# Kernel optimization log

Hardware: AMD Instinct MI355X
Metric: run time of the kernel (lower is better)

## Reference

```python
import jax, jax.numpy as jnp
import numpy as np

NEG_INF = -9e15
ALPHA = 0.2  # LeakyReLU negative slope
OUT_FEATURES = 128


def setup_inputs() -> dict:
    key = jax.random.key(0)
    k1, k2, k3, k4 = jax.random.split(key, 4)
    B, N, F_in, F_out = 4, 4096, 256, OUT_FEATURES
    h = jax.random.normal(k1, (B, N, F_in), dtype=jnp.float32)
    adj = jax.random.randint(k2, (B, N, N), 0, 2, dtype=jnp.int32)
    W = jax.random.normal(k3, (F_in, F_out), dtype=jnp.float32) * 0.07
    a = jax.random.normal(k4, (2 * F_out, 1), dtype=jnp.float32) * 0.1
    return {"h": h, "adj": adj, "W": W, "a": a}


def reference(h, adj, W, a):
    # Wh: (B, N, F_out)
    Wh = jnp.einsum('bni,io->bno', h, W)
    a1 = a[:OUT_FEATURES, 0]   # (F_out,)
    a2 = a[OUT_FEATURES:, 0]   # (F_out,)
    Wh1 = Wh @ a1              # (B, N)
    Wh2 = Wh @ a2              # (B, N)
    e = Wh1[:, :, None] + Wh2[:, None, :]          # (B, N, N)
    e = jnp.where(e >= 0, e, ALPHA * e)             # LeakyReLU
    e = jnp.where(adj > 0, e, NEG_INF)              # adjacency mask
    attention = jax.nn.softmax(e, axis=-1)          # (B, N, N)
    # dropout omitted: reference runs in eval mode (training=False)
    h_prime = jnp.einsum('bnm,bmo->bno', attention, Wh)
    return jax.nn.elu(h_prime)  # concat=True
```

## Files before the change

kernel.cpp:

```cpp
#include <hip/hip_runtime.h>
#include <hip/hip_bf16.h>
#include <math.h>

typedef __attribute__((ext_vector_type(4))) float  f32x4;
typedef __attribute__((ext_vector_type(4))) int    i32x4;
typedef __attribute__((ext_vector_type(8))) short  s16x8;
typedef __attribute__((ext_vector_type(4))) short  s16x4;
typedef __attribute__((ext_vector_type(8))) __bf16 bf16x8;

#define LOG2E 1.4426950408889634f

__device__ __forceinline__ short f32_to_bf16_rne(float f) {
    unsigned u = __builtin_bit_cast(unsigned, f);
    u += 0x7fffu + ((u >> 16) & 1u);
    return (short)(u >> 16);
}
__device__ __forceinline__ int pack2_bf16(float f0, float f1) {
    unsigned u0 = __builtin_bit_cast(unsigned, f0) + 0x8000u;
    unsigned u1 = __builtin_bit_cast(unsigned, f1) + 0x8000u;
    return (int)((u0 >> 16) | (u1 & 0xffff0000u));
}
__device__ __forceinline__ bf16x8 as_bf16x8(s16x8 v) {
    return __builtin_bit_cast(bf16x8, v);
}
__device__ __forceinline__ bf16x8 as_bf16x8(i32x4 v) {
    return __builtin_bit_cast(bf16x8, v);
}

__global__ void k0_wt(const float* __restrict__ W, short* __restrict__ WT) {
    int g = blockIdx.x * 256 + threadIdx.x;
    int col = g >> 6;
    int k0 = (g & 63) * 4;
    s16x4 v;
    #pragma unroll
    for (int i = 0; i < 4; ++i) v[i] = f32_to_bf16_rne(W[(k0 + i) * 128 + col]);
    *(s16x4*)(WT + col * 256 + k0) = v;
}

__global__ __launch_bounds__(256, 2) void k1_gemm(
    const float* __restrict__ h, const float* __restrict__ a,
    const short* __restrict__ WT,
    short* __restrict__ WhT, float* __restrict__ Wh1p, float* __restrict__ Tp)
{
    int l = threadIdx.x & 63;
    int w = threadIdx.x >> 6;
    int gw = blockIdx.x * 4 + w;
    int r0 = gw * 16;
    int lm = l & 15, q = l >> 4;

    f32x4 acc[8];
    #pragma unroll
    for (int ct = 0; ct < 8; ++ct) acc[ct] = (f32x4)0.0f;

    const float* hrow = h + (long)(r0 + lm) * 256;
    for (int kb = 0; kb < 8; ++kb) {
        int kbase = kb * 32 + q * 8;
        f32x4 h0 = *(const f32x4*)(hrow + kbase);
        f32x4 h1 = *(const f32x4*)(hrow + kbase + 4);
        s16x8 af;
        #pragma unroll
        for (int j = 0; j < 4; ++j) af[j] = f32_to_bf16_rne(h0[j]);
        #pragma unroll
        for (int j = 0; j < 4; ++j) af[4 + j] = f32_to_bf16_rne(h1[j]);
        bf16x8 afb = as_bf16x8(af);
        #pragma unroll
        for (int ct = 0; ct < 8; ++ct) {
            s16x8 bf = *(const s16x8*)(WT + (ct * 16 + lm) * 256 + kbase);
            acc[ct] = __builtin_amdgcn_mfma_f32_16x16x32_bf16(afb, as_bf16x8(bf), acc[ct], 0, 0, 0);
        }
    }

    int b = r0 >> 12;
    int nb = r0 & 4095;
    float p1[4] = {0.f, 0.f, 0.f, 0.f}, p2[4] = {0.f, 0.f, 0.f, 0.f};
    #pragma unroll
    for (int ct = 0; ct < 8; ++ct) {
        int col = ct * 16 + lm;
        float a1c = a[col], a2c = a[128 + col];
        s16x4 vv;
        #pragma unroll
        for (int r = 0; r < 4; ++r) {
            float v = acc[ct][r];
            p1[r] += v * a1c;
            p2[r] += v * a2c;
            vv[r] = f32_to_bf16_rne(v);
        }
        *(s16x4*)(WhT + ((long)(b * 128 + col) * 4096 + nb + q * 4)) = vv;
    }
    #pragma unroll
    for (int off = 1; off < 16; off <<= 1) {
        #pragma unroll
        for (int r = 0; r < 4; ++r) {
            p1[r] += __shfl_xor(p1[r], off);
            p2[r] += __shfl_xor(p2[r], off);
        }
    }
    if (lm == 0) {
        #pragma unroll
        for (int r = 0; r < 4; ++r) {
            int row = r0 + q * 4 + r;
            Wh1p[row] = LOG2E * p1[r];
            Tp[row]   = LOG2E * p2[r];
        }
    }
}

__global__ void k2_tmax(const float* __restrict__ Tp, float* __restrict__ Tmax) {
    __shared__ float red[256];
    int b = blockIdx.x, t = threadIdx.x;
    float mx = -1e30f;
    for (int i = 0; i < 16; ++i) mx = fmaxf(mx, Tp[b * 4096 + t + i * 256]);
    red[t] = mx;
    __syncthreads();
    for (int s = 128; s > 0; s >>= 1) {
        if (t < s) red[t] = fmaxf(red[t], red[t + s]);
        __syncthreads();
    }
    if (t == 0) Tmax[b] = red[0];
}

template <int SPLIT>
__global__ __launch_bounds__(256, 2) void k3_attn(
    const int* __restrict__ adj, const short* __restrict__ WhT,
    const float* __restrict__ Wh1p, const float* __restrict__ Tp,
    const float* __restrict__ Tmax,
    float* __restrict__ U, float* __restrict__ Z)
{
    const int MSLICE = 4096 / SPLIT;
    const int MTILES = MSLICE / 128;
    __shared__ __align__(16) short tile[2][128 * 128];
    __shared__ __align__(16) float tps[4096 / SPLIT];

    int l = threadIdx.x & 63, w = threadIdx.x >> 6;
    int lm = l & 15, q = l >> 4;
    int bid = blockIdx.x;
    int mh = bid & (SPLIT - 1);
    int rg = (bid / SPLIT) & 63;
    int b  = bid / (SPLIT * 64);
    int n0 = rg * 64;
    int mbase = mh * MSLICE;

    int n_lane = n0 + w * 16 + lm;
    float sp = Wh1p[b * 4096 + n_lane];
    float xm = sp + Tmax[b];
    float Mrow = fmaxf(xm, 0.2f * xm);

    const int*   adjrow = adj + ((long)(b * 4096 + n_lane) << 12) + q * 8;
    const short* whtb   = WhT + (long)b * 128 * 4096;
    const float* tpsq   = tps + q * 8;

    {
        const float* tg = Tp + b * 4096 + mbase;
        int i0 = threadIdx.x * 4;
        *(f32x4*)(tps + i0)        = *(const f32x4*)(tg + i0);
        *(f32x4*)(tps + i0 + 1024) = *(const f32x4*)(tg + i0 + 1024);
    }

    f32x4 acc[8];
    #pragma unroll
    for (int ct = 0; ct < 8; ++ct) acc[ct] = (f32x4)0.0f;
    float z = 0.0f;

    auto stage = [&](short* dst, int m0) {
        int colw = w * 32;
        #pragma unroll
        for (int j = 0; j < 8; ++j) {
            int cb = colw + j * 4;
            int col = cb + q;
            int gch = lm ^ (col & 7);
            const short* gp = whtb + (long)col * 4096 + m0 + gch * 8;
            __builtin_amdgcn_global_load_lds(
                (const __attribute__((address_space(1))) void*)gp,
                (__attribute__((address_space(3))) void*)(dst + cb * 128), 16, 0, 0);
        }
    };
    auto ldadj = [&](i32x4* aj, int m0) {
        #pragma unroll
        for (int ks = 0; ks < 4; ++ks) {
            aj[2 * ks]     = *(const i32x4*)(adjrow + m0 + ks * 32);
            aj[2 * ks + 1] = *(const i32x4*)(adjrow + m0 + ks * 32 + 4);
        }
    };
    auto compute = [&](const short* buf, const i32x4* aj, int mrel) {
        #pragma unroll
        for (int ks = 0; ks < 4; ++ks) {
            f32x4 t0 = *(const f32x4*)(tpsq + mrel + ks * 32);
            f32x4 t1 = *(const f32x4*)(tpsq + mrel + ks * 32 + 4);
            i32x4 pk;
            float zs = 0.0f;
            #pragma unroll
            for (int half = 0; half < 2; ++half) {
                i32x4 a4 = aj[2 * ks + half];
                f32x4 t4 = half ? t1 : t0;
                float wv[4];
                #pragma unroll
                for (int j = 0; j < 4; ++j) {
                    float y = sp + t4[j];
                    float e = fmaxf(y, 0.2f * y) - Mrow;
                    float v = __builtin_amdgcn_exp2f(e);
                    v = (a4[j] != 0) ? v : 0.0f;
                    zs += v; wv[j] = v;
                }
                pk[half * 2]     = pack2_bf16(wv[0], wv[1]);
                pk[half * 2 + 1] = pack2_bf16(wv[2], wv[3]);
            }
            z += zs;
            bf16x8 ab = as_bf16x8(pk);
            #pragma unroll
            for (int ct = 0; ct < 8; ++ct) {
                int col = ct * 16 + lm;
                int pos = (ks * 4 + q) ^ (col & 7);
                s16x8 bf = *(const s16x8*)(buf + col * 128 + pos * 8);
                acc[ct] = __builtin_amdgcn_mfma_f32_16x16x32_bf16(ab, as_bf16x8(bf), acc[ct], 0, 0, 0);
            }
        }
    };

    i32x4 ajA[8], ajB[8];
    stage(tile[0], mbase);
    ldadj(ajA, mbase);
    __syncthreads();

    #pragma unroll 1
    for (int t = 0; t < MTILES; t += 2) {
        int r1 = (t + 1) & (MTILES - 1);
        stage(tile[1], mbase + r1 * 128);
        ldadj(ajB, mbase + r1 * 128);
        __builtin_amdgcn_sched_barrier(0);
        compute(tile[0], ajA, t * 128);
        __syncthreads();
        int r2 = (t + 2) & (MTILES - 1);
        stage(tile[0], mbase + r2 * 128);
        ldadj(ajA, mbase + r2 * 128);
        __builtin_amdgcn_sched_barrier(0);
        compute(tile[1], ajB, r1 * 128);
        __syncthreads();
    }

    z += __shfl_xor(z, 16);
    z += __shfl_xor(z, 32);

    int slice = b * SPLIT + mh;
    if (l < 16) Z[slice * 4096 + n0 + w * 16 + lm] = z;
    float* ub = U + ((long)slice * 4096 + n0 + w * 16) * 128;
    #pragma unroll
    for (int ct = 0; ct < 8; ++ct) {
        int col = ct * 16 + lm;
        #pragma unroll
        for (int r = 0; r < 4; ++r)
            ub[(q * 4 + r) * 128 + col] = acc[ct][r];
    }
}

__global__ void k4_combine(const float* __restrict__ U, const float* __restrict__ Z,
                           float* __restrict__ out) {
    long g = (long)blockIdx.x * 256 + threadIdx.x;
    long off = g * 4;
    long nf = off >> 7;
    int b = (int)(nf >> 12), n = (int)(nf & 4095), col = (int)(off & 127);
    long base0 = ((long)(b * 2) * 4096 + n) * 128 + col;
    f32x4 u0 = *(const f32x4*)(U + base0);
    f32x4 u1 = *(const f32x4*)(U + base0 + (long)4096 * 128);
    float zz = Z[(b * 2) * 4096 + n] + Z[(b * 2 + 1) * 4096 + n];
    f32x4 v;
    #pragma unroll
    for (int i = 0; i < 4; ++i) {
        float x = (u0[i] + u1[i]) / zz;
        v[i] = (x > 0.f) ? x : (expf(x) - 1.0f);
    }
    *(f32x4*)(out + off) = v;
}

extern "C" void kernel_launch(void* const* d_in, const int* in_sizes, int n_in,
                              void* d_out, int out_size, void* d_ws, size_t ws_size,
                              hipStream_t stream) {
    const float* h   = (const float*)d_in[0];
    const int*   adj = (const int*)d_in[1];
    const float* W   = (const float*)d_in[2];
    const float* a   = (const float*)d_in[3];
    float* out = (float*)d_out;

    char* ws = (char*)d_ws;
    short* WhT  = (short*)ws;
    short* WT   = (short*)(ws + 4194304);
    float* Wh1p = (float*)(ws + 4259840);
    float* Tp   = (float*)(ws + 4325376);
    float* Tmax = (float*)(ws + 4390912);
    float* U    = (float*)(ws + 4391168);
    float* Z    = (float*)(ws + 4391168 + 16777216);

    k0_wt<<<32, 256, 0, stream>>>(W, WT);
    k1_gemm<<<256, 256, 0, stream>>>(h, a, WT, WhT, Wh1p, Tp);
    k2_tmax<<<4, 256, 0, stream>>>(Tp, Tmax);
    k3_attn<2><<<512, 256, 0, stream>>>(adj, WhT, Wh1p, Tp, Tmax, U, Z);
    k4_combine<<<2048, 256, 0, stream>>>(U, Z, out);
    (void)in_sizes; (void)n_in; (void)out_size; (void)ws_size;
}
```

Baseline: 404.7 us.

## Pre-pack adjacency matrix into bitmasks before attention kernel

```diff
diff --git a/kernel.cpp b/kernel.cpp
--- a/kernel.cpp
+++ b/kernel.cpp
@@ -4,6 +4,7 @@
 
 typedef __attribute__((ext_vector_type(4))) float  f32x4;
 typedef __attribute__((ext_vector_type(4))) int    i32x4;
+typedef __attribute__((ext_vector_type(4))) unsigned u32x4;
 typedef __attribute__((ext_vector_type(8))) short  s16x8;
 typedef __attribute__((ext_vector_type(4))) short  s16x4;
 typedef __attribute__((ext_vector_type(8))) __bf16 bf16x8;
@@ -25,6 +26,20 @@
 }
 __device__ __forceinline__ bf16x8 as_bf16x8(i32x4 v) {
     return __builtin_bit_cast(bf16x8, v);
+}
+
+__global__ void k_pack(const int* __restrict__ adj, unsigned* __restrict__ bits) {
+    long t = (long)blockIdx.x * 256 + threadIdx.x;
+    const int* src = adj + t * 32;
+    unsigned m = 0;
+    #pragma unroll
+    for (int c = 0; c < 8; ++c) {
+        i32x4 v = *(const i32x4*)(src + c * 4);
+        #pragma unroll
+        for (int j = 0; j < 4; ++j)
+            m |= (v[j] != 0) ? (1u << (c * 4 + j)) : 0u;
+    }
+    bits[t] = m;
 }
 
 __global__ void k0_wt(const float* __restrict__ W, short* __restrict__ WT) {
@@ -121,7 +136,7 @@
 
 template <int SPLIT>
 __global__ __launch_bounds__(256, 2) void k3_attn(
-    const int* __restrict__ adj, const short* __restrict__ WhT,
+    const unsigned* __restrict__ bits, const short* __restrict__ WhT,
     const float* __restrict__ Wh1p, const float* __restrict__ Tp,
     const float* __restrict__ Tmax,
     float* __restrict__ U, float* __restrict__ Z)
@@ -145,7 +160,7 @@
     float xm = sp + Tmax[b];
     float Mrow = fmaxf(xm, 0.2f * xm);
 
-    const int*   adjrow = adj + ((long)(b * 4096 + n_lane) << 12) + q * 8;
+    const unsigned* bitrow = bits + ((long)(b * 4096 + n_lane)) * 128 + mbase / 32;
     const short* whtb   = WhT + (long)b * 128 * 4096;
     const float* tpsq   = tps + q * 8;
 
@@ -174,23 +189,16 @@
                 (__attribute__((address_space(3))) void*)(dst + cb * 128), 16, 0, 0);
         }
     };
-    auto ldadj = [&](i32x4* aj, int m0) {
-        #pragma unroll
-        for (int ks = 0; ks < 4; ++ks) {
-            aj[2 * ks]     = *(const i32x4*)(adjrow + m0 + ks * 32);
-            aj[2 * ks + 1] = *(const i32x4*)(adjrow + m0 + ks * 32 + 4);
-        }
-    };
-    auto compute = [&](const short* buf, const i32x4* aj, int mrel) {
+    auto compute = [&](const short* buf, u32x4 bw, int mrel) {
         #pragma unroll
         for (int ks = 0; ks < 4; ++ks) {
             f32x4 t0 = *(const f32x4*)(tpsq + mrel + ks * 32);
             f32x4 t1 = *(const f32x4*)(tpsq + mrel + ks * 32 + 4);
+            unsigned mq = bw[ks] >> (q * 8);
             i32x4 pk;
             float zs = 0.0f;
             #pragma unroll
             for (int half = 0; half < 2; ++half) {
-                i32x4 a4 = aj[2 * ks + half];
                 f32x4 t4 = half ? t1 : t0;
                 float wv[4];
                 #pragma unroll
@@ -198,7 +206,7 @@
                     float y = sp + t4[j];
                     float e = fmaxf(y, 0.2f * y) - Mrow;
                     float v = __builtin_amdgcn_exp2f(e);
-                    v = (a4[j] != 0) ? v : 0.0f;
+                    v = (mq & (1u << (half * 4 + j))) ? v : 0.0f;
                     zs += v; wv[j] = v;
                 }
                 pk[half * 2]     = pack2_bf16(wv[0], wv[1]);
@@ -216,24 +224,24 @@
         }
     };
 
-    i32x4 ajA[8], ajB[8];
+    u32x4 bwA, bwB;
     stage(tile[0], mbase);
-    ldadj(ajA, mbase);
+    bwA = *(const u32x4*)(bitrow);
     __syncthreads();
 
     #pragma unroll 1
     for (int t = 0; t < MTILES; t += 2) {
         int r1 = (t + 1) & (MTILES - 1);
         stage(tile[1], mbase + r1 * 128);
-        ldadj(ajB, mbase + r1 * 128);
+        bwB = *(const u32x4*)(bitrow + r1 * 4);
         __builtin_amdgcn_sched_barrier(0);
-        compute(tile[0], ajA, t * 128);
+        compute(tile[0], bwA, t * 128);
         __syncthreads();
         int r2 = (t + 2) & (MTILES - 1);
         stage(tile[0], mbase + r2 * 128);
-        ldadj(ajA, mbase + r2 * 128);
+        bwA = *(const u32x4*)(bitrow + r2 * 4);
         __builtin_amdgcn_sched_barrier(0);
-        compute(tile[1], ajB, r1 * 128);
+        compute(tile[1], bwB, r1 * 128);
         __syncthreads();
     }
 
@@ -281,18 +289,20 @@
     float* out = (float*)d_out;
 
     char* ws = (char*)d_ws;
-    short* WhT  = (short*)ws;
-    short* WT   = (short*)(ws + 4194304);
-    float* Wh1p = (float*)(ws + 4259840);
-    float* Tp   = (float*)(ws + 4325376);
-    float* Tmax = (float*)(ws + 4390912);
-    float* U    = (float*)(ws + 4391168);
-    float* Z    = (float*)(ws + 4391168 + 16777216);
-
+    short*    WhT  = (short*)ws;
+    short*    WT   = (short*)(ws + 4194304);
+    float*    Wh1p = (float*)(ws + 4259840);
+    float*    Tp   = (float*)(ws + 4325376);
+    float*    Tmax = (float*)(ws + 4390912);
+    float*    U    = (float*)(ws + 4391168);
+    float*    Z    = (float*)(ws + 4391168 + 16777216);
+    unsigned* bits = (unsigned*)(ws + 4391168 + 16777216 + 131072);
+
+    k_pack<<<8192, 256, 0, stream>>>(adj, bits);
     k0_wt<<<32, 256, 0, stream>>>(W, WT);
     k1_gemm<<<256, 256, 0, stream>>>(h, a, WT, WhT, Wh1p, Tp);
     k2_tmax<<<4, 256, 0, stream>>>(Tp, Tmax);
-    k3_attn<2><<<512, 256, 0, stream>>>(adj, WhT, Wh1p, Tp, Tmax, U, Z);
+    k3_attn<2><<<512, 256, 0, stream>>>(bits, WhT, Wh1p, Tp, Tmax, U, Z);
     k4_combine<<<2048, 256, 0, stream>>>(U, Z, out);
     (void)in_sizes; (void)n_in; (void)out_size; (void)ws_size;
 }
```

Result: slower. 438.2 us (+8.3%).
